# Performance work log

Hardware: AMD Instinct MI355X
Metric: run time of the kernel (lower is better)

## Reference

```python
import jax, jax.numpy as jnp
import numpy as np

B, T, IN, OUT, H = 1024, 25, 96, 96, 2048


def setup_inputs() -> dict:
    key = jax.random.key(0)
    ks = jax.random.split(key, 16)
    s = 0.05  # small init scale to keep gates in linear-ish region
    return {
        "input": jax.random.normal(ks[0], (B, IN), jnp.float32),
        "future_poses": jax.random.normal(ks[1], (B, T, OUT), jnp.float32),
        "hiddens": jax.random.normal(ks[2], (2, B, H), jnp.float32) * s,
        "W_ih0": jax.random.normal(ks[3], (3 * H, IN), jnp.float32) * s,
        "W_hh0": jax.random.normal(ks[4], (3 * H, H), jnp.float32) * s,
        "b_ih0": jax.random.normal(ks[5], (3 * H,), jnp.float32) * s,
        "b_hh0": jax.random.normal(ks[6], (3 * H,), jnp.float32) * s,
        "W_ih1": jax.random.normal(ks[7], (3 * H, H), jnp.float32) * s,
        "W_hh1": jax.random.normal(ks[8], (3 * H, H), jnp.float32) * s,
        "b_ih1": jax.random.normal(ks[9], (3 * H,), jnp.float32) * s,
        "b_hh1": jax.random.normal(ks[10], (3 * H,), jnp.float32) * s,
        "W_fc": jax.random.normal(ks[11], (OUT, H), jnp.float32) * s,
        "b_fc": jax.random.normal(ks[12], (OUT,), jnp.float32) * s,
        "teacher_forcing_rate": 0,
    }


def gru_cell(x, h, W_ih, W_hh, b_ih, b_hh):
    # PyTorch nn.GRUCell math; gate order [r, z, n]
    gi = x @ W_ih.T + b_ih
    gh = h @ W_hh.T + b_hh
    i_r, i_z, i_n = jnp.split(gi, 3, axis=-1)
    h_r, h_z, h_n = jnp.split(gh, 3, axis=-1)
    r = jax.nn.sigmoid(i_r + h_r)
    z = jax.nn.sigmoid(i_z + h_z)
    n = jnp.tanh(i_n + r * h_n)
    return (1.0 - z) * n + z * h


def reference(input, future_poses, hiddens, W_ih0, W_hh0, b_ih0, b_hh0,
              W_ih1, W_hh1, b_ih1, b_hh1, W_fc, b_fc, teacher_forcing_rate):
    # dropout p=0.0 (eval) -> identity; teacher_forcing_rate=0 -> always
    def step(carry, _):
        dec_in, h0, h1 = carry
        h0 = gru_cell(dec_in, h0, W_ih0, W_hh0, b_ih0, b_hh0)
        h1 = gru_cell(h0, h1, W_ih1, W_hh1, b_ih1, b_hh1)
        out = jax.nn.sigmoid(h1 @ W_fc.T + b_fc)  # [B, OUT]
        dec_in = jax.lax.stop_gradient(out)       # torch .detach()
        return (dec_in, h0, h1), out

    carry0 = (input, hiddens[0], hiddens[1])
    _, outs = jax.lax.scan(step, carry0, None, length=T)  # [T, B, OUT]
    return jnp.transpose(outs, (1, 0, 2))  # [B, T, OUT]
```

## Files before the change

### kernel.cpp

```cpp
#include <hip/hip_runtime.h>
#include <stdint.h>

typedef __bf16 bf16;
typedef __attribute__((ext_vector_type(8))) __bf16 bf16x8;
typedef __attribute__((ext_vector_type(4))) float f32x4;

#define GRU_H 2048
#define ODIM 96
#define PADX 128
#define BATCH 1024
#define TSTEPS 25

__device__ __forceinline__ float sigm(float x) { return 1.f / (1.f + __expf(-x)); }

__device__ __forceinline__ void gload16(const void* g, void* l) {
  __builtin_amdgcn_global_load_lds((const __attribute__((address_space(1))) uint32_t*)g,
                                   (__attribute__((address_space(3))) uint32_t*)l, 16, 0, 0);
}

__global__ void k_cvt(const float* __restrict__ s, bf16* __restrict__ d, int n) {
  int stride = gridDim.x * blockDim.x;
  for (int i = blockIdx.x * blockDim.x + threadIdx.x; i < n; i += stride)
    d[i] = (bf16)s[i];
}

__global__ void k_cvt_pad(const float* __restrict__ s, bf16* __restrict__ d,
                          int rows, int cin, int cout) {
  int n = rows * cout;
  int stride = gridDim.x * blockDim.x;
  for (int i = blockIdx.x * blockDim.x + threadIdx.x; i < n; i += stride) {
    int r = i / cout, c = i - r * cout;
    d[i] = (c < cin) ? (bf16)s[r * cin + c] : (bf16)0.f;
  }
}

__global__ void k_init_h(const float* __restrict__ s, float* __restrict__ hf,
                         bf16* __restrict__ hb, int n) {
  int stride = gridDim.x * blockDim.x;
  for (int i = blockIdx.x * blockDim.x + threadIdx.x; i < n; i += stride) {
    float v = s[i];
    hf[i] = v;
    hb[i] = (bf16)v;
  }
}

__global__ __launch_bounds__(256) void k_gru(
    const bf16* __restrict__ xb, int kx,
    const bf16* __restrict__ hb,
    const bf16* __restrict__ wih,
    const bf16* __restrict__ whh,
    const float* __restrict__ bih, const float* __restrict__ bhh,
    const float* __restrict__ hprevf,
    float* __restrict__ hnewf, bf16* __restrict__ hnewb) {
  __shared__ alignas(16) char sm[2][32768];

  const int tid = threadIdx.x;
  const int l = tid & 63;
  const int wn = tid >> 6;
  const int wb = tid & ~63;
  const int bn0 = blockIdx.x * 64;
  const int bm0 = blockIdx.y * 64;
  const int lm = l >> 4, ln = l & 15;
  char* sm0 = &sm[0][0];

  const int S1 = GRU_H / 64;
  const int S2 = kx / 64;

  f32x4 accR[4] = {};
  f32x4 accZ[4] = {};
  f32x4 accNH[4] = {};
  f32x4 accNI[4] = {};

  auto stage = [&](int lb2, const bf16* __restrict__ A, const bf16* __restrict__ W,
                   int K, int k0) {
    char* sb = sm0 + lb2;
#pragma unroll
    for (int it = 0; it < 2; ++it) {
      int c = it * 256 + tid;
      int row = c >> 3, pos = c & 7, slot = pos ^ (row & 7);
      gload16(A + (size_t)(bm0 + row) * K + k0 + slot * 8,
              sb + ((it * 256 + wb) << 4));
    }
#pragma unroll
    for (int it = 0; it < 6; ++it) {
      int c = it * 256 + tid;
      int row = c >> 3, pos = c & 7, slot = pos ^ (row & 7);
      int g = row >> 6, r = row & 63;
      gload16(W + (size_t)(g * GRU_H + bn0 + r) * K + k0 + slot * 8,
              sb + 8192 + ((it * 256 + wb) << 4));
    }
  };

  auto computeStep = [&](int lb2, f32x4 (&accN)[4]) {
    const char* bp = sm0 + lb2;
#pragma unroll
    for (int kf = 0; kf < 2; ++kf) {
      bf16x8 af[4];
#pragma unroll
      for (int mf = 0; mf < 4; ++mf) {
        int row = mf * 16 + ln;
        int pos = (kf * 4 + lm) ^ (row & 7);
        af[mf] = *(const bf16x8*)(bp + row * 128 + (pos << 4));
      }
#pragma unroll
      for (int g = 0; g < 3; ++g) {
        int row = g * 64 + wn * 16 + ln;
        int pos = (kf * 4 + lm) ^ (row & 7);
        bf16x8 bq = *(const bf16x8*)(bp + 8192 + row * 128 + (pos << 4));
        f32x4* accG = (g == 0) ? accR : (g == 1) ? accZ : accN;
#pragma unroll
        for (int mf = 0; mf < 4; ++mf)
          accG[mf] = __builtin_amdgcn_mfma_f32_16x16x32_bf16(af[mf], bq, accG[mf], 0, 0, 0);
      }
    }
  };

  stage(0, hb, whh, GRU_H, 0);
  asm volatile("s_waitcnt vmcnt(0)\ns_barrier" ::: "memory");

  int lb = 0;
  for (int s = 0; s < S1; ++s) {
    if (s + 1 < S1) stage(lb ^ 32768, hb, whh, GRU_H, (s + 1) * 64);
    else            stage(lb ^ 32768, xb, wih, kx, 0);
    computeStep(lb, accNH);
    asm volatile("s_waitcnt vmcnt(0) lgkmcnt(0)\ns_barrier" ::: "memory");
    lb ^= 32768;
  }
  for (int s = 0; s < S2; ++s) {
    if (s + 1 < S2) {
      stage(lb ^ 32768, xb, wih, kx, (s + 1) * 64);
      computeStep(lb, accNI);
      asm volatile("s_waitcnt vmcnt(0) lgkmcnt(0)\ns_barrier" ::: "memory");
      lb ^= 32768;
    } else {
      computeStep(lb, accNI);
    }
  }

  {
    int j = bn0 + wn * 16 + ln;
    float br = bih[j] + bhh[j];
    float bz = bih[GRU_H + j] + bhh[GRU_H + j];
    float bin = bih[2 * GRU_H + j];
    float bhn = bhh[2 * GRU_H + j];
#pragma unroll
    for (int mf = 0; mf < 4; ++mf) {
#pragma unroll
      for (int rr = 0; rr < 4; ++rr) {
        int m = bm0 + mf * 16 + lm * 4 + rr;
        size_t idx = (size_t)m * GRU_H + j;
        float hp = hprevf[idx];
        float rg = sigm(accR[mf][rr] + br);
        float zg = sigm(accZ[mf][rr] + bz);
        float ng = tanhf(accNI[mf][rr] + bin + rg * (accNH[mf][rr] + bhn));
        float hn = (1.f - zg) * ng + zg * hp;
        hnewf[idx] = hn;
        hnewb[idx] = (bf16)hn;
      }
    }
  }
}

__global__ __launch_bounds__(256, 1) void k_fc_part(const bf16* __restrict__ h1b,
                                                    const bf16* __restrict__ wfc,
                                                    float* __restrict__ part) {
  const int kc = blockIdx.x;
  const int mt = blockIdx.y;
  const int l = threadIdx.x & 63, w = threadIdx.x >> 6;
  const int lm = l >> 4, ln = l & 15;
  const int m0 = mt * 64 + w * 16;
  const int k0 = kc * 128;
  f32x4 acc[6] = {};
#pragma unroll
  for (int kf = 0; kf < 4; ++kf) {
    bf16x8 a = *(const bf16x8*)&h1b[(size_t)(m0 + ln) * GRU_H + k0 + kf * 32 + lm * 8];
#pragma unroll
    for (int nf = 0; nf < 6; ++nf) {
      bf16x8 b = *(const bf16x8*)&wfc[(size_t)(nf * 16 + ln) * GRU_H + k0 + kf * 32 + lm * 8];
      acc[nf] = __builtin_amdgcn_mfma_f32_16x16x32_bf16(a, b, acc[nf], 0, 0, 0);
    }
  }
  float* base = part + (size_t)kc * (BATCH * ODIM);
#pragma unroll
  for (int nf = 0; nf < 6; ++nf)
#pragma unroll
    for (int rr = 0; rr < 4; ++rr)
      base[(size_t)(m0 + lm * 4 + rr) * ODIM + nf * 16 + ln] = acc[nf][rr];
}

__global__ void k_fc_red(const float* __restrict__ part, const float* __restrict__ bfc,
                         float* __restrict__ dout, bf16* __restrict__ decb, int t) {
  int i = blockIdx.x * blockDim.x + threadIdx.x;
  if (i >= BATCH * ODIM) return;
  int m = i / ODIM, n = i - m * ODIM;
  float s = bfc[n];
#pragma unroll
  for (int kc = 0; kc < 16; ++kc) s += part[(size_t)kc * (BATCH * ODIM) + i];
  s = sigm(s);
  dout[(size_t)m * (TSTEPS * ODIM) + t * ODIM + n] = s;
  decb[m * PADX + n] = (bf16)s;
}

extern "C" void kernel_launch(void* const* d_in, const int* in_sizes, int n_in,
                              void* d_out, int out_size, void* d_ws, size_t ws_size,
                              hipStream_t stream) {
  const float* input   = (const float*)d_in[0];
  const float* hiddens = (const float*)d_in[2];
  const float* W_ih0   = (const float*)d_in[3];
  const float* W_hh0   = (const float*)d_in[4];
  const float* b_ih0   = (const float*)d_in[5];
  const float* b_hh0   = (const float*)d_in[6];
  const float* W_ih1   = (const float*)d_in[7];
  const float* W_hh1   = (const float*)d_in[8];
  const float* b_ih1   = (const float*)d_in[9];
  const float* b_hh1   = (const float*)d_in[10];
  const float* W_fc    = (const float*)d_in[11];
  const float* b_fc    = (const float*)d_in[12];
  float* out = (float*)d_out;

  char* p = (char*)d_ws;
  auto take = [&](size_t n) { char* q = p; p += (n + 255) & ~(size_t)255; return q; };
  bf16* wih0b = (bf16*)take((size_t)3 * GRU_H * PADX * 2);
  bf16* whh0b = (bf16*)take((size_t)3 * GRU_H * GRU_H * 2);
  bf16* wih1b = (bf16*)take((size_t)3 * GRU_H * GRU_H * 2);
  bf16* whh1b = (bf16*)take((size_t)3 * GRU_H * GRU_H * 2);
  bf16* wfcb  = (bf16*)take((size_t)ODIM * GRU_H * 2);
  bf16* decb  = (bf16*)take((size_t)BATCH * PADX * 2);
  float* h0f[2], *h1f[2];
  bf16* h0b[2], *h1b[2];
  h0f[0] = (float*)take((size_t)BATCH * GRU_H * 4);
  h0f[1] = (float*)take((size_t)BATCH * GRU_H * 4);
  h1f[0] = (float*)take((size_t)BATCH * GRU_H * 4);
  h1f[1] = (float*)take((size_t)BATCH * GRU_H * 4);
  h0b[0] = (bf16*)take((size_t)BATCH * GRU_H * 2);
  h0b[1] = (bf16*)take((size_t)BATCH * GRU_H * 2);
  h1b[0] = (bf16*)take((size_t)BATCH * GRU_H * 2);
  h1b[1] = (bf16*)take((size_t)BATCH * GRU_H * 2);
  float* fcpart = (float*)take((size_t)16 * BATCH * ODIM * 4);

  k_cvt_pad<<<768, 256, 0, stream>>>(W_ih0, wih0b, 3 * GRU_H, ODIM, PADX);
  k_cvt<<<2048, 256, 0, stream>>>(W_hh0, whh0b, 3 * GRU_H * GRU_H);
  k_cvt<<<2048, 256, 0, stream>>>(W_ih1, wih1b, 3 * GRU_H * GRU_H);
  k_cvt<<<2048, 256, 0, stream>>>(W_hh1, whh1b, 3 * GRU_H * GRU_H);
  k_cvt<<<192, 256, 0, stream>>>(W_fc, wfcb, ODIM * GRU_H);
  k_cvt_pad<<<512, 256, 0, stream>>>(input, decb, BATCH, ODIM, PADX);
  k_init_h<<<2048, 256, 0, stream>>>(hiddens, h0f[0], h0b[0], BATCH * GRU_H);
  k_init_h<<<2048, 256, 0, stream>>>(hiddens + (size_t)BATCH * GRU_H, h1f[0], h1b[0], BATCH * GRU_H);

  int cur = 0;
  for (int t = 0; t < TSTEPS; ++t) {
    int nxt = cur ^ 1;
    k_gru<<<dim3(32, 16), 256, 0, stream>>>(decb, PADX, h0b[cur], wih0b, whh0b,
                                            b_ih0, b_hh0, h0f[cur], h0f[nxt], h0b[nxt]);
    k_gru<<<dim3(32, 16), 256, 0, stream>>>(h0b[nxt], GRU_H, h1b[cur], wih1b, whh1b,
                                            b_ih1, b_hh1, h1f[cur], h1f[nxt], h1b[nxt]);
    k_fc_part<<<dim3(16, 16), 256, 0, stream>>>(h1b[nxt], wfcb, fcpart);
    k_fc_red<<<384, 256, 0, stream>>>(fcpart, b_fc, out, decb, t);
    cur = nxt;
  }
}
```

Before: 2.874 ms.

## Use 128-row GRU tiles with 8 waves and a triple-buffered load pipeline

Each GRU GEMM block now covers 128 batch rows instead of 64, using 512 threads (2x4 waves) on a grid half as tall. Doubling the row tile halves how often the weight tiles are re-fetched. The double-buffered K loop becomes a three-stage ring, unrolled by three: loads are issued two steps ahead, with a partial vmcnt wait and s_setprio raised around the MFMA work. Global source pointers are also precomputed once. In exchange, LDS use grows to 120KB per block, and with one block per CU there may be fewer waves in flight to hide latency.

```diff
diff --git a/kernel.cpp b/kernel.cpp
--- a/kernel.cpp
+++ b/kernel.cpp
@@ -44,7 +44,7 @@
   }
 }
 
-__global__ __launch_bounds__(256) void k_gru(
+__global__ __launch_bounds__(512, 1) void k_gru(
     const bf16* __restrict__ xb, int kx,
     const bf16* __restrict__ hb,
     const bf16* __restrict__ wih,
@@ -52,53 +52,64 @@
     const float* __restrict__ bih, const float* __restrict__ bhh,
     const float* __restrict__ hprevf,
     float* __restrict__ hnewf, bf16* __restrict__ hnewb) {
-  __shared__ alignas(16) char sm[2][32768];
+  __shared__ alignas(16) char sm[3][40960];
 
   const int tid = threadIdx.x;
   const int l = tid & 63;
-  const int wn = tid >> 6;
+  const int w = tid >> 6;
+  const int wm = w & 1, wn = w >> 1;
   const int wb = tid & ~63;
   const int bn0 = blockIdx.x * 64;
-  const int bm0 = blockIdx.y * 64;
+  const int bm0 = blockIdx.y * 128;
   const int lm = l >> 4, ln = l & 15;
   char* sm0 = &sm[0][0];
 
   const int S1 = GRU_H / 64;
   const int S2 = kx / 64;
+  const int S = S1 + S2;
 
   f32x4 accR[4] = {};
   f32x4 accZ[4] = {};
   f32x4 accNH[4] = {};
   f32x4 accNI[4] = {};
 
-  auto stage = [&](int lb2, const bf16* __restrict__ A, const bf16* __restrict__ W,
-                   int K, int k0) {
-    char* sb = sm0 + lb2;
-#pragma unroll
-    for (int it = 0; it < 2; ++it) {
-      int c = it * 256 + tid;
-      int row = c >> 3, pos = c & 7, slot = pos ^ (row & 7);
-      gload16(A + (size_t)(bm0 + row) * K + k0 + slot * 8,
-              sb + ((it * 256 + wb) << 4));
-    }
-#pragma unroll
-    for (int it = 0; it < 6; ++it) {
-      int c = it * 256 + tid;
-      int row = c >> 3, pos = c & 7, slot = pos ^ (row & 7);
-      int g = row >> 6, r = row & 63;
-      gload16(W + (size_t)(g * GRU_H + bn0 + r) * K + k0 + slot * 8,
-              sb + 8192 + ((it * 256 + wb) << 4));
-    }
-  };
-
-  auto computeStep = [&](int lb2, f32x4 (&accN)[4]) {
-    const char* bp = sm0 + lb2;
+  const bf16* pAhh[2]; const bf16* pAih[2]; int ldsA[2];
+  const bf16* pWhh[3]; const bf16* pWih[3]; int ldsB[3];
+#pragma unroll
+  for (int i = 0; i < 2; ++i) {
+    int c = i * 512 + tid, row = c >> 3, slot = (c & 7) ^ (row & 7);
+    pAhh[i] = hb + (size_t)(bm0 + row) * GRU_H + slot * 8;
+    pAih[i] = xb + (size_t)(bm0 + row) * kx + slot * 8;
+    ldsA[i] = (i * 512 + wb) << 4;
+  }
+#pragma unroll
+  for (int i = 0; i < 3; ++i) {
+    int c = i * 512 + tid, row = c >> 3, slot = (c & 7) ^ (row & 7);
+    int g = row >> 6, r = row & 63;
+    pWhh[i] = whh + (size_t)(g * GRU_H + bn0 + r) * GRU_H + slot * 8;
+    pWih[i] = wih + (size_t)(g * GRU_H + bn0 + r) * kx + slot * 8;
+    ldsB[i] = 16384 + ((i * 512 + wb) << 4);
+  }
+
+  auto stageP = [&](const bf16* const (&pa)[2], const bf16* const (&pw)[3],
+                    int koff, char* sb) {
+#pragma unroll
+    for (int i = 0; i < 2; ++i) gload16(pa[i] + koff, sb + ldsA[i]);
+#pragma unroll
+    for (int i = 0; i < 3; ++i) gload16(pw[i] + koff, sb + ldsB[i]);
+  };
+  auto stageSel = [&](int sp, char* sb) {
+    if (sp < S1) stageP(pAhh, pWhh, sp * 64, sb);
+    else         stageP(pAih, pWih, (sp - S1) * 64, sb);
+  };
+
+  auto computeStep = [&](const char* bp, f32x4 (&accN)[4]) {
 #pragma unroll
     for (int kf = 0; kf < 2; ++kf) {
       bf16x8 af[4];
 #pragma unroll
       for (int mf = 0; mf < 4; ++mf) {
-        int row = mf * 16 + ln;
+        int row = wm * 64 + mf * 16 + ln;
         int pos = (kf * 4 + lm) ^ (row & 7);
         af[mf] = *(const bf16x8*)(bp + row * 128 + (pos << 4));
       }
@@ -106,7 +117,7 @@
       for (int g = 0; g < 3; ++g) {
         int row = g * 64 + wn * 16 + ln;
         int pos = (kf * 4 + lm) ^ (row & 7);
-        bf16x8 bq = *(const bf16x8*)(bp + 8192 + row * 128 + (pos << 4));
+        bf16x8 bq = *(const bf16x8*)(bp + 16384 + row * 128 + (pos << 4));
         f32x4* accG = (g == 0) ? accR : (g == 1) ? accZ : accN;
 #pragma unroll
         for (int mf = 0; mf < 4; ++mf)
@@ -115,27 +126,28 @@
     }
   };
 
-  stage(0, hb, whh, GRU_H, 0);
-  asm volatile("s_waitcnt vmcnt(0)\ns_barrier" ::: "memory");
-
-  int lb = 0;
-  for (int s = 0; s < S1; ++s) {
-    if (s + 1 < S1) stage(lb ^ 32768, hb, whh, GRU_H, (s + 1) * 64);
-    else            stage(lb ^ 32768, xb, wih, kx, 0);
-    computeStep(lb, accNH);
-    asm volatile("s_waitcnt vmcnt(0) lgkmcnt(0)\ns_barrier" ::: "memory");
-    lb ^= 32768;
-  }
-  for (int s = 0; s < S2; ++s) {
-    if (s + 1 < S2) {
-      stage(lb ^ 32768, xb, wih, kx, (s + 1) * 64);
-      computeStep(lb, accNI);
-      asm volatile("s_waitcnt vmcnt(0) lgkmcnt(0)\ns_barrier" ::: "memory");
-      lb ^= 32768;
-    } else {
-      computeStep(lb, accNI);
-    }
-  }
+  auto body = [&](int s, char* bufR, char* bufW) {
+    asm volatile("s_waitcnt vmcnt(5) lgkmcnt(0)\ns_barrier" ::: "memory");
+    if (s + 2 < S) stageSel(s + 2, bufW);
+    __builtin_amdgcn_s_setprio(1);
+    if (s < S1) computeStep(bufR, accNH);
+    else        computeStep(bufR, accNI);
+    __builtin_amdgcn_s_setprio(0);
+  };
+
+  stageSel(0, sm0);
+  stageSel(1, sm0 + 40960);
+
+  const int SM1 = S - 1;
+  for (int s = 0; s < SM1; s += 3) {
+    body(s + 0, sm0,         sm0 + 81920);
+    body(s + 1, sm0 + 40960, sm0);
+    body(s + 2, sm0 + 81920, sm0 + 40960);
+  }
+  asm volatile("s_waitcnt vmcnt(0) lgkmcnt(0)\ns_barrier" ::: "memory");
+  __builtin_amdgcn_s_setprio(1);
+  computeStep(sm0, accNI);
+  __builtin_amdgcn_s_setprio(0);
 
   {
     int j = bn0 + wn * 16 + ln;
@@ -147,7 +159,7 @@
     for (int mf = 0; mf < 4; ++mf) {
 #pragma unroll
       for (int rr = 0; rr < 4; ++rr) {
-        int m = bm0 + mf * 16 + lm * 4 + rr;
+        int m = bm0 + wm * 64 + mf * 16 + lm * 4 + rr;
         size_t idx = (size_t)m * GRU_H + j;
         float hp = hprevf[idx];
         float rg = sigm(accR[mf][rr] + br);
@@ -250,10 +262,10 @@
   int cur = 0;
   for (int t = 0; t < TSTEPS; ++t) {
     int nxt = cur ^ 1;
-    k_gru<<<dim3(32, 16), 256, 0, stream>>>(decb, PADX, h0b[cur], wih0b, whh0b,
-                                            b_ih0, b_hh0, h0f[cur], h0f[nxt], h0b[nxt]);
-    k_gru<<<dim3(32, 16), 256, 0, stream>>>(h0b[nxt], GRU_H, h1b[cur], wih1b, whh1b,
-                                            b_ih1, b_hh1, h1f[cur], h1f[nxt], h1b[nxt]);
+    k_gru<<<dim3(32, 8), 512, 0, stream>>>(decb, PADX, h0b[cur], wih0b, whh0b,
+                                           b_ih0, b_hh0, h0f[cur], h0f[nxt], h0b[nxt]);
+    k_gru<<<dim3(32, 8), 512, 0, stream>>>(h0b[nxt], GRU_H, h1b[cur], wih1b, whh1b,
+                                           b_ih1, b_hh1, h1f[cur], h1f[nxt], h1b[nxt]);
     k_fc_part<<<dim3(16, 16), 256, 0, stream>>>(h1b[nxt], wfcb, fcpart);
     k_fc_red<<<384, 256, 0, stream>>>(fcpart, b_fc, out, decb, t);
     cur = nxt;
```

Measured after the change: 2.566 ms. 1.12x faster.

## Triple-buffer GRU GEMM with BK=32 and two loads in flight

Applied to the files above, without the earlier changes.

Reworks the GRU gate GEMM main loop. It halves the K tile to 32, uses three LDS buffers so two stages of global-to-LDS loads are in flight, and waits with vmcnt(4) instead of draining all loads before every barrier. Global and LDS addresses are now precomputed once with a new swizzle for 64-byte rows, the hh and ih phases are merged into a single loop, and MFMA sections are wrapped in s_setprio. The aim is to hide memory latency better and cut per-iteration address math. The cost is twice as many barriers and iterations per K, with fewer MFMAs to amortize each one.

```diff
diff --git a/kernel.cpp b/kernel.cpp
--- a/kernel.cpp
+++ b/kernel.cpp
@@ -52,90 +52,93 @@
     const float* __restrict__ bih, const float* __restrict__ bhh,
     const float* __restrict__ hprevf,
     float* __restrict__ hnewf, bf16* __restrict__ hnewb) {
-  __shared__ alignas(16) char sm[2][32768];
+  __shared__ alignas(16) char sm[3][16384];
 
   const int tid = threadIdx.x;
   const int l = tid & 63;
   const int wn = tid >> 6;
-  const int wb = tid & ~63;
   const int bn0 = blockIdx.x * 64;
   const int bm0 = blockIdx.y * 64;
   const int lm = l >> 4, ln = l & 15;
-  char* sm0 = &sm[0][0];
-
-  const int S1 = GRU_H / 64;
-  const int S2 = kx / 64;
+  char* const b0 = &sm[0][0];
+  char* const b1 = &sm[1][0];
+  char* const b2 = &sm[2][0];
+
+  const int S1 = GRU_H / 32;
+  const int S2 = kx / 32;
+  const int S = S1 + S2;
 
   f32x4 accR[4] = {};
   f32x4 accZ[4] = {};
   f32x4 accNH[4] = {};
   f32x4 accNI[4] = {};
 
-  auto stage = [&](int lb2, const bf16* __restrict__ A, const bf16* __restrict__ W,
-                   int K, int k0) {
-    char* sb = sm0 + lb2;
-#pragma unroll
-    for (int it = 0; it < 2; ++it) {
-      int c = it * 256 + tid;
-      int row = c >> 3, pos = c & 7, slot = pos ^ (row & 7);
-      gload16(A + (size_t)(bm0 + row) * K + k0 + slot * 8,
-              sb + ((it * 256 + wb) << 4));
-    }
-#pragma unroll
-    for (int it = 0; it < 6; ++it) {
-      int c = it * 256 + tid;
-      int row = c >> 3, pos = c & 7, slot = pos ^ (row & 7);
-      int g = row >> 6, r = row & 63;
-      gload16(W + (size_t)(g * GRU_H + bn0 + r) * K + k0 + slot * 8,
-              sb + 8192 + ((it * 256 + wb) << 4));
+  const int r0 = tid >> 2;
+  const int kg = ((((tid & 3) - (tid >> 3)) & 3)) * 8;
+  const bf16* pAhh = hb + (size_t)(bm0 + r0) * GRU_H + kg;
+  const bf16* pAih = xb + (size_t)(bm0 + r0) * kx + kg;
+  const bf16* pWhh[3]; const bf16* pWih[3]; int ldsB[3];
+#pragma unroll
+  for (int g = 0; g < 3; ++g) {
+    pWhh[g] = whh + (size_t)(g * GRU_H + bn0 + r0) * GRU_H + kg;
+    pWih[g] = wih + (size_t)(g * GRU_H + bn0 + r0) * kx + kg;
+    ldsB[g] = 4096 + ((g * 256 + (tid & ~63)) << 4);
+  }
+  const int ldsA = (tid & ~63) << 4;
+
+  auto stageSel = [&](int sp, char* sb) {
+    if (sp < S1) {
+      int k0 = sp * 32;
+      gload16(pAhh + k0, sb + ldsA);
+#pragma unroll
+      for (int g = 0; g < 3; ++g) gload16(pWhh[g] + k0, sb + ldsB[g]);
+    } else {
+      int k0 = (sp - S1) * 32;
+      gload16(pAih + k0, sb + ldsA);
+#pragma unroll
+      for (int g = 0; g < 3; ++g) gload16(pWih[g] + k0, sb + ldsB[g]);
     }
   };
 
-  auto computeStep = [&](int lb2, f32x4 (&accN)[4]) {
-    const char* bp = sm0 + lb2;
-#pragma unroll
-    for (int kf = 0; kf < 2; ++kf) {
-      bf16x8 af[4];
-#pragma unroll
-      for (int mf = 0; mf < 4; ++mf) {
-        int row = mf * 16 + ln;
-        int pos = (kf * 4 + lm) ^ (row & 7);
-        af[mf] = *(const bf16x8*)(bp + row * 128 + (pos << 4));
-      }
-#pragma unroll
-      for (int g = 0; g < 3; ++g) {
-        int row = g * 64 + wn * 16 + ln;
-        int pos = (kf * 4 + lm) ^ (row & 7);
-        bf16x8 bq = *(const bf16x8*)(bp + 8192 + row * 128 + (pos << 4));
-        f32x4* accG = (g == 0) ? accR : (g == 1) ? accZ : accN;
-#pragma unroll
-        for (int mf = 0; mf < 4; ++mf)
-          accG[mf] = __builtin_amdgcn_mfma_f32_16x16x32_bf16(af[mf], bq, accG[mf], 0, 0, 0);
-      }
+  const int pos = ((lm + (ln >> 1)) & 3) << 4;
+
+  auto computeStep = [&](const char* bp, f32x4 (&accN)[4]) {
+    bf16x8 af[4];
+#pragma unroll
+    for (int mf = 0; mf < 4; ++mf)
+      af[mf] = *(const bf16x8*)(bp + (mf * 16 + ln) * 64 + pos);
+#pragma unroll
+    for (int g = 0; g < 3; ++g) {
+      bf16x8 bq = *(const bf16x8*)(bp + 4096 + (g * 64 + wn * 16 + ln) * 64 + pos);
+      f32x4* accG = (g == 0) ? accR : (g == 1) ? accZ : accN;
+#pragma unroll
+      for (int mf = 0; mf < 4; ++mf)
+        accG[mf] = __builtin_amdgcn_mfma_f32_16x16x32_bf16(af[mf], bq, accG[mf], 0, 0, 0);
     }
   };
 
-  stage(0, hb, whh, GRU_H, 0);
-  asm volatile("s_waitcnt vmcnt(0)\ns_barrier" ::: "memory");
-
-  int lb = 0;
-  for (int s = 0; s < S1; ++s) {
-    if (s + 1 < S1) stage(lb ^ 32768, hb, whh, GRU_H, (s + 1) * 64);
-    else            stage(lb ^ 32768, xb, wih, kx, 0);
-    computeStep(lb, accNH);
-    asm volatile("s_waitcnt vmcnt(0) lgkmcnt(0)\ns_barrier" ::: "memory");
-    lb ^= 32768;
-  }
-  for (int s = 0; s < S2; ++s) {
-    if (s + 1 < S2) {
-      stage(lb ^ 32768, xb, wih, kx, (s + 1) * 64);
-      computeStep(lb, accNI);
-      asm volatile("s_waitcnt vmcnt(0) lgkmcnt(0)\ns_barrier" ::: "memory");
-      lb ^= 32768;
-    } else {
-      computeStep(lb, accNI);
-    }
-  }
+  auto body = [&](int s, char* bufR, char* bufW, bool last) {
+    if (!last) asm volatile("s_waitcnt vmcnt(4) lgkmcnt(0)" ::: "memory");
+    else       asm volatile("s_waitcnt vmcnt(0) lgkmcnt(0)" ::: "memory");
+    __builtin_amdgcn_s_barrier();
+    if (s + 2 < S) stageSel(s + 2, bufW);
+    __builtin_amdgcn_s_setprio(1);
+    if (s < S1) computeStep(bufR, accNH);
+    else        computeStep(bufR, accNI);
+    __builtin_amdgcn_s_setprio(0);
+  };
+
+  stageSel(0, b0);
+  stageSel(1, b1);
+
+  int s = 0;
+  for (; s + 2 < S; s += 3) {
+    body(s + 0, b0, b2, false);
+    body(s + 1, b1, b0, false);
+    body(s + 2, b2, b1, false);
+  }
+  body(s + 0, b0, b2, false);
+  body(s + 1, b1, b0, true);
 
   {
     int j = bn0 + wn * 16 + ln;
```

Measured after the change: 3.673 ms. 27.8% more time.
